# Performance work log

Measured on AMD Instinct MI355X. Metric: run time of the kernel, lower is better.

The kernel has to match this reference:

```python
import jax, jax.numpy as jnp
import numpy as np

B, H, KVH, D, HID = 32, 32, 8, 128, 4096
WIN, MAX_SEQ = 4096, 4096
START_POS = 3000
CURRENT_POS = 3000  # circular index into sliding-window cache

def nearest_32(n):
    return ((n + 31) // 32) * 32

PAD_L = min(nearest_32(START_POS + 1), WIN)  # 3008

def setup_inputs() -> dict:
    key = jax.random.key(0)
    k1, k2, k3 = jax.random.split(key, 3)
    x = jax.random.normal(k1, (1, 1, B, HID), jnp.float32) * 0.02
    wqkv = jax.random.normal(k2, (HID, (H + 2 * KVH) * D), jnp.float32) * 0.02
    wo = jax.random.normal(k3, (HID, HID), jnp.float32) * 0.02
    cache_k = jnp.zeros((B, KVH, WIN, D), jnp.float32)
    cache_v = jnp.zeros((B, KVH, WIN, D), jnp.float32)
    # RoPE tables (rotate-half convention, cos/sin of shape [max_seq_len, head_dim])
    inv_freq = 1.0 / (10000.0 ** (jnp.arange(0, D, 2, dtype=jnp.float32) / D))
    t = jnp.arange(MAX_SEQ, dtype=jnp.float32)
    freqs = jnp.outer(t, inv_freq)                      # [S, D/2]
    emb = jnp.concatenate([freqs, freqs], axis=-1)      # [S, D]
    cos_cached = jnp.cos(emb)
    sin_cached = jnp.sin(emb)
    # additive mask: 0 for valid cache positions (<= start_pos), -1e9 for tile padding
    pos = jnp.arange(PAD_L)
    row = jnp.where(pos <= START_POS, 0.0, -1e9).astype(jnp.float32)
    attn_mask = jnp.broadcast_to(row, (1, H, B, PAD_L))
    return {"x": x, "wqkv": wqkv, "wo": wo, "cache_k": cache_k, "cache_v": cache_v,
            "cos_cached": cos_cached, "sin_cached": sin_cached, "attn_mask": attn_mask,
            "start_pos": START_POS, "current_pos": CURRENT_POS}

def _rotate_half(u):
    return jnp.concatenate([-u[..., D // 2:], u[..., :D // 2]], axis=-1)

def reference(x, wqkv, wo, cache_k, cache_v, cos_cached, sin_cached, attn_mask,
              start_pos, current_pos):
    # fused QKV projection: x is (1,1,B,HID) decode token
    xqkv = x[0, 0] @ wqkv                               # [B, (H+2KVH)*D]
    q = xqkv[:, :H * D].reshape(B, H, D)
    k = xqkv[:, H * D:(H + KVH) * D].reshape(B, KVH, D)
    v = xqkv[:, (H + KVH) * D:].reshape(B, KVH, D)
    # RoPE at position start_pos
    cos = cos_cached[start_pos]                         # [D]
    sin = sin_cached[start_pos]
    q = q * cos + _rotate_half(q) * sin
    k = k * cos + _rotate_half(k) * sin
    # sliding-window circular KV-cache update at current_pos
    cache_k = cache_k.at[:, :, current_pos, :].set(k)
    cache_v = cache_v.at[:, :, current_pos, :].set(v)
    keys = cache_k[:, :, :PAD_L, :]                     # [B, KVH, L, D]
    vals = cache_v[:, :, :PAD_L, :]
    # grouped-query attention
    G = H // KVH
    qg = q.reshape(B, KVH, G, D)
    scores = jnp.einsum('bkgd,bkld->bkgl', qg, keys) / jnp.sqrt(jnp.float32(D))
    mask = jnp.transpose(attn_mask[0], (1, 0, 2)).reshape(B, KVH, G, PAD_L)
    probs = jax.nn.softmax(scores + mask, axis=-1)
    ctx = jnp.einsum('bkgl,bkld->bkgd', probs, vals).reshape(B, H * D)
    dense = ctx @ wo                                    # [B, HID]
    return dense.reshape(1, 1, B, HID)
```

## Files before the change

### kernel.cpp

```cpp
#include <hip/hip_runtime.h>
#include <hip/hip_bf16.h>

#define B 32
#define H 32
#define KVH 8
#define D 128
#define HID 4096
#define NQKV 6144
#define WIN 4096
#define PADL_MAX 3008
#define KS1 16
#define KS4 32

#define OFF_XT   0
#define OFF_P1   131072
#define OFF_QR   (OFF_P1 + KS1*B*NQKV)
#define OFF_KR   (OFF_QR + B*H*D)
#define OFF_VV   (OFF_KR + B*KVH*D)
#define OFF_CTXT (OFF_VV + B*KVH*D)
#define OFF_P4   (OFF_CTXT + B*H*D)

__global__ __launch_bounds__(1024) void k_transpose(const float* __restrict__ x,
                                                    float* __restrict__ xT) {
  __shared__ float t[32][33];
  const int k0 = blockIdx.x * 32;
  const int r = threadIdx.x >> 5, i = threadIdx.x & 31;
  t[r][i] = x[r * HID + k0 + i];
  __syncthreads();
  xT[(k0 + r) * 32 + i] = t[i][r];
}

__global__ __launch_bounds__(256) void k_qkv(const float* __restrict__ xT,
                                             const float* __restrict__ wqkv,
                                             float* __restrict__ P1) {
  __shared__ float xs[256 * 32];
  const int ct = blockIdx.x, ks = blockIdx.y;
  const int tid = threadIdx.x;
  const int col = ct * 256 + tid;
  const int k0 = ks * 256;
  for (int i = tid; i < 256 * 32; i += 256) xs[i] = xT[k0 * 32 + i];
  __syncthreads();
  float acc[32];
#pragma unroll
  for (int b = 0; b < 32; ++b) acc[b] = 0.f;
  const float* wp = wqkv + (size_t)k0 * NQKV + col;
  for (int kk = 0; kk < 256; ++kk) {
    const float w = wp[(size_t)kk * NQKV];
    const float* xr = xs + kk * 32;
#pragma unroll
    for (int b = 0; b < 32; b += 4) {
      const float4 xv = *(const float4*)(xr + b);
      acc[b + 0] = fmaf(xv.x, w, acc[b + 0]);
      acc[b + 1] = fmaf(xv.y, w, acc[b + 1]);
      acc[b + 2] = fmaf(xv.z, w, acc[b + 2]);
      acc[b + 3] = fmaf(xv.w, w, acc[b + 3]);
    }
  }
  float* op = P1 + (size_t)ks * (B * NQKV) + col;
#pragma unroll
  for (int b = 0; b < 32; ++b) op[(size_t)b * NQKV] = acc[b];
}

__global__ __launch_bounds__(256) void k_rope_reduce(const float* __restrict__ P1,
                                                     const float* __restrict__ cosc,
                                                     const float* __restrict__ sinc,
                                                     const int* __restrict__ spp,
                                                     float* __restrict__ qr,
                                                     float* __restrict__ kr,
                                                     float* __restrict__ vv) {
  const int t = blockIdx.x * 256 + threadIdx.x;
  const int sp = *spp;
  if (t < B * (H + KVH) * 64) {
    const int b = t / ((H + KVH) * 64);
    const int r = t % ((H + KVH) * 64);
    const int h = r >> 6;
    const int d = r & 63;
    const int base = b * NQKV + h * D + d;
    float sA = 0.f, sB = 0.f;
#pragma unroll
    for (int s = 0; s < KS1; ++s) {
      sA += P1[(size_t)s * (B * NQKV) + base];
      sB += P1[(size_t)s * (B * NQKV) + base + 64];
    }
    const float cA = cosc[sp * D + d],     snA = sinc[sp * D + d];
    const float cB = cosc[sp * D + d + 64], snB = sinc[sp * D + d + 64];
    const float oA = sA * cA - sB * snA;
    const float oB = sB * cB + sA * snB;
    if (h < H) {
      qr[b * (H * D) + h * D + d] = oA;
      qr[b * (H * D) + h * D + d + 64] = oB;
    } else {
      const int kvh = h - H;
      kr[b * (KVH * D) + kvh * D + d] = oA;
      kr[b * (KVH * D) + kvh * D + d + 64] = oB;
    }
  } else {
    const int i = t - B * (H + KVH) * 64;
    const int b = i >> 10, c = i & 1023;
    float s = 0.f;
#pragma unroll
    for (int ss = 0; ss < KS1; ++ss)
      s += P1[(size_t)ss * (B * NQKV) + b * NQKV + (H + KVH) * D + c];
    vv[i] = s;
  }
}

__global__ __launch_bounds__(1024) void k_attn(const float* __restrict__ cache_k,
                                               const float* __restrict__ cache_v,
                                               const float* __restrict__ qr,
                                               const float* __restrict__ kr,
                                               const float* __restrict__ vv,
                                               const int* __restrict__ spp,
                                               const int* __restrict__ cpp,
                                               float* __restrict__ ctxT) {
  __shared__ float sl[4 * PADL_MAX];
  __shared__ float red[16];
  __shared__ float mg[4], inv[4];
  const int b = blockIdx.x >> 3, kv = blockIdx.x & 7;
  const int sp = *spp, cp = *cpp;
  const int L = sp;
  const int tid = threadIdx.x;
  const int wave = tid >> 6, lane = tid & 63;
  const int half = lane >> 5, j = lane & 31;
  const size_t kvbase = (size_t)(b * KVH + kv) * WIN * D;
  const float scale = 0.08838834764831845f;

  float4 ql[4];
#pragma unroll
  for (int g = 0; g < 4; ++g) {
    float4 q4 = *(const float4*)(qr + b * (H * D) + (kv * 4 + g) * D + 4 * j);
    ql[g] = make_float4(q4.x * scale, q4.y * scale, q4.z * scale, q4.w * scale);
  }

  const int NP = L / 2;
  for (int p = wave; p <= NP; p += 16) {
    const int l = 2 * p + half;
    if (l <= L) {
      const float* kp = (l == cp) ? (kr + (b * KVH + kv) * D)
                                  : (cache_k + kvbase + (size_t)l * D);
      const float4 k4 = *(const float4*)(kp + 4 * j);
#pragma unroll
      for (int g = 0; g < 4; ++g) {
        float s = ql[g].x * k4.x + ql[g].y * k4.y + ql[g].z * k4.z + ql[g].w * k4.w;
#pragma unroll
        for (int m = 1; m <= 16; m <<= 1) s += __shfl_xor(s, m);
        if (j == 0) sl[g * PADL_MAX + l] = s;
      }
    }
  }
  __syncthreads();

  {
    const int g = tid >> 8, i = tid & 255, w4 = (tid >> 6) & 3;
    float m = -1e30f;
    for (int l = i; l <= L; l += 256) m = fmaxf(m, sl[g * PADL_MAX + l]);
#pragma unroll
    for (int mm = 1; mm <= 32; mm <<= 1) m = fmaxf(m, __shfl_xor(m, mm));
    if (lane == 0) red[g * 4 + w4] = m;
    __syncthreads();
    if (i == 0)
      mg[g] = fmaxf(fmaxf(red[g * 4], red[g * 4 + 1]),
                    fmaxf(red[g * 4 + 2], red[g * 4 + 3]));
    __syncthreads();
    const float mgv = mg[g];
    float psum = 0.f;
    for (int l = i; l <= L; l += 256) {
      const float e = __expf(sl[g * PADL_MAX + l] - mgv);
      sl[g * PADL_MAX + l] = e;
      psum += e;
    }
#pragma unroll
    for (int mm = 1; mm <= 32; mm <<= 1) psum += __shfl_xor(psum, mm);
    if (lane == 0) red[g * 4 + w4] = psum;
    __syncthreads();
    if (i == 0)
      inv[g] = 1.f / (red[g * 4] + red[g * 4 + 1] + red[g * 4 + 2] + red[g * 4 + 3]);
    __syncthreads();
  }

  float o[4][4];
#pragma unroll
  for (int g = 0; g < 4; ++g)
#pragma unroll
    for (int c = 0; c < 4; ++c) o[g][c] = 0.f;
  for (int p = wave; p <= NP; p += 16) {
    const int l = 2 * p + half;
    if (l <= L) {
      const float* vp = (l == cp) ? (vv + (b * KVH + kv) * D)
                                  : (cache_v + kvbase + (size_t)l * D);
      const float4 v4 = *(const float4*)(vp + 4 * j);
#pragma unroll
      for (int g = 0; g < 4; ++g) {
        const float e = sl[g * PADL_MAX + l];
        o[g][0] = fmaf(e, v4.x, o[g][0]);
        o[g][1] = fmaf(e, v4.y, o[g][1]);
        o[g][2] = fmaf(e, v4.z, o[g][2]);
        o[g][3] = fmaf(e, v4.w, o[g][3]);
      }
    }
  }
#pragma unroll
  for (int g = 0; g < 4; ++g)
#pragma unroll
    for (int c = 0; c < 4; ++c) o[g][c] += __shfl_xor(o[g][c], 32);

  __syncthreads();
  if (lane < 32) {
#pragma unroll
    for (int g = 0; g < 4; ++g)
      *(float4*)&sl[wave * 512 + g * 128 + 4 * j] =
          make_float4(o[g][0], o[g][1], o[g][2], o[g][3]);
  }
  __syncthreads();
  if (tid < 512) {
    const int g = tid >> 7, d = tid & 127;
    float a = 0.f;
#pragma unroll
    for (int w = 0; w < 16; ++w) a += sl[w * 512 + g * 128 + d];
    a *= inv[g];
    ctxT[(size_t)((kv * 4 + g) * D + d) * B + b] = a;
  }
}

__global__ __launch_bounds__(256) void k_out(const float* __restrict__ ctxT,
                                             const float* __restrict__ wo,
                                             float* __restrict__ P4) {
  __shared__ float cs[128 * 32];
  const int ct = blockIdx.x, ks = blockIdx.y;
  const int tid = threadIdx.x;
  const int col = ct * 256 + tid;
  const int k0 = ks * 128;
  for (int i = tid; i < 128 * 32; i += 256) cs[i] = ctxT[k0 * 32 + i];
  __syncthreads();
  float acc[32];
#pragma unroll
  for (int b = 0; b < 32; ++b) acc[b] = 0.f;
  const float* wp = wo + (size_t)k0 * HID + col;
  for (int kk = 0; kk < 128; ++kk) {
    const float w = wp[(size_t)kk * HID];
    const float* xr = cs + kk * 32;
#pragma unroll
    for (int b = 0; b < 32; b += 4) {
      const float4 xv = *(const float4*)(xr + b);
      acc[b + 0] = fmaf(xv.x, w, acc[b + 0]);
      acc[b + 1] = fmaf(xv.y, w, acc[b + 1]);
      acc[b + 2] = fmaf(xv.z, w, acc[b + 2]);
      acc[b + 3] = fmaf(xv.w, w, acc[b + 3]);
    }
  }
  float* op = P4 + (size_t)ks * (B * HID) + col;
#pragma unroll
  for (int b = 0; b < 32; ++b) op[(size_t)b * HID] = acc[b];
}

__global__ __launch_bounds__(256) void k_final(const float* __restrict__ P4,
                                               float* __restrict__ out) {
  const int e = blockIdx.x * 256 + threadIdx.x;
  float s = 0.f;
#pragma unroll
  for (int ss = 0; ss < KS4; ++ss) s += P4[(size_t)ss * (B * HID) + e];
  out[e] = s;
}

extern "C" void kernel_launch(void* const* d_in, const int* in_sizes, int n_in,
                              void* d_out, int out_size, void* d_ws, size_t ws_size,
                              hipStream_t stream) {
  const float* x       = (const float*)d_in[0];
  const float* wqkv    = (const float*)d_in[1];
  const float* wo      = (const float*)d_in[2];
  const float* cache_k = (const float*)d_in[3];
  const float* cache_v = (const float*)d_in[4];
  const float* cosc    = (const float*)d_in[5];
  const float* sinc    = (const float*)d_in[6];
  const int* spp       = (const int*)d_in[8];
  const int* cpp       = (const int*)d_in[9];
  float* ws = (float*)d_ws;

  k_transpose<<<128, 1024, 0, stream>>>(x, ws + OFF_XT);
  k_qkv<<<dim3(24, 16), 256, 0, stream>>>(ws + OFF_XT, wqkv, ws + OFF_P1);
  k_rope_reduce<<<448, 256, 0, stream>>>(ws + OFF_P1, cosc, sinc, spp,
                                         ws + OFF_QR, ws + OFF_KR, ws + OFF_VV);
  k_attn<<<256, 1024, 0, stream>>>(cache_k, cache_v, ws + OFF_QR, ws + OFF_KR,
                                   ws + OFF_VV, spp, cpp, ws + OFF_CTXT);
  k_out<<<dim3(16, 32), 256, 0, stream>>>(ws + OFF_CTXT, wo, ws + OFF_P4);
  k_final<<<512, 256, 0, stream>>>(ws + OFF_P4, (float*)d_out);
}
```

Before: 1.178 ms.

## Drop transpose kernel, read activations directly in GEMVs, restructure QK scoring

Removes the separate x transpose kernel and the shared-memory staging in the QKV and output projections. Each thread now computes two columns with float2 weight loads and reads activations straight from global memory as wave-uniform broadcast loads. The split-K count for QKV is raised to 32 and the grids are resized to match. The attention QK phase is changed so 8 lanes cooperate per key row with q held in registers, which cuts the shuffle reduction from 5 steps to 3 per score. The trade-off is more partial-sum traffic from the larger split-K and more register pressure from the 2x32 accumulators.

```diff
diff --git a/kernel.cpp b/kernel.cpp
--- a/kernel.cpp
+++ b/kernel.cpp
@@ -9,56 +9,39 @@
 #define NQKV 6144
 #define WIN 4096
 #define PADL_MAX 3008
-#define KS1 16
+#define KS1 32
 #define KS4 32
 
-#define OFF_XT   0
-#define OFF_P1   131072
+#define OFF_P1   0
 #define OFF_QR   (OFF_P1 + KS1*B*NQKV)
 #define OFF_KR   (OFF_QR + B*H*D)
 #define OFF_VV   (OFF_KR + B*KVH*D)
-#define OFF_CTXT (OFF_VV + B*KVH*D)
-#define OFF_P4   (OFF_CTXT + B*H*D)
-
-__global__ __launch_bounds__(1024) void k_transpose(const float* __restrict__ x,
-                                                    float* __restrict__ xT) {
-  __shared__ float t[32][33];
-  const int k0 = blockIdx.x * 32;
-  const int r = threadIdx.x >> 5, i = threadIdx.x & 31;
-  t[r][i] = x[r * HID + k0 + i];
-  __syncthreads();
-  xT[(k0 + r) * 32 + i] = t[i][r];
-}
-
-__global__ __launch_bounds__(256) void k_qkv(const float* __restrict__ xT,
+#define OFF_CTX  (OFF_VV + B*KVH*D)
+#define OFF_P4   (OFF_CTX + B*H*D)
+
+__global__ __launch_bounds__(256) void k_qkv(const float* __restrict__ x,
                                              const float* __restrict__ wqkv,
                                              float* __restrict__ P1) {
-  __shared__ float xs[256 * 32];
-  const int ct = blockIdx.x, ks = blockIdx.y;
-  const int tid = threadIdx.x;
-  const int col = ct * 256 + tid;
-  const int k0 = ks * 256;
-  for (int i = tid; i < 256 * 32; i += 256) xs[i] = xT[k0 * 32 + i];
-  __syncthreads();
-  float acc[32];
-#pragma unroll
-  for (int b = 0; b < 32; ++b) acc[b] = 0.f;
+  const int ks = blockIdx.y;
+  const int col = blockIdx.x * 512 + threadIdx.x * 2;
+  const int k0 = ks * 128;
+  float2 acc[32];
+#pragma unroll
+  for (int b = 0; b < 32; ++b) acc[b] = make_float2(0.f, 0.f);
   const float* wp = wqkv + (size_t)k0 * NQKV + col;
-  for (int kk = 0; kk < 256; ++kk) {
-    const float w = wp[(size_t)kk * NQKV];
-    const float* xr = xs + kk * 32;
-#pragma unroll
-    for (int b = 0; b < 32; b += 4) {
-      const float4 xv = *(const float4*)(xr + b);
-      acc[b + 0] = fmaf(xv.x, w, acc[b + 0]);
-      acc[b + 1] = fmaf(xv.y, w, acc[b + 1]);
-      acc[b + 2] = fmaf(xv.z, w, acc[b + 2]);
-      acc[b + 3] = fmaf(xv.w, w, acc[b + 3]);
+  for (int kk = 0; kk < 128; ++kk) {
+    const float2 w2 = *(const float2*)(wp + (size_t)kk * NQKV);
+    const int xi = k0 + kk;
+#pragma unroll
+    for (int b = 0; b < 32; ++b) {
+      const float xv = x[b * HID + xi];
+      acc[b].x = fmaf(xv, w2.x, acc[b].x);
+      acc[b].y = fmaf(xv, w2.y, acc[b].y);
     }
   }
   float* op = P1 + (size_t)ks * (B * NQKV) + col;
 #pragma unroll
-  for (int b = 0; b < 32; ++b) op[(size_t)b * NQKV] = acc[b];
+  for (int b = 0; b < 32; ++b) *(float2*)(op + (size_t)b * NQKV) = acc[b];
 }
 
 __global__ __launch_bounds__(256) void k_rope_reduce(const float* __restrict__ P1,
@@ -82,7 +65,7 @@
       sA += P1[(size_t)s * (B * NQKV) + base];
       sB += P1[(size_t)s * (B * NQKV) + base + 64];
     }
-    const float cA = cosc[sp * D + d],     snA = sinc[sp * D + d];
+    const float cA = cosc[sp * D + d],      snA = sinc[sp * D + d];
     const float cB = cosc[sp * D + d + 64], snB = sinc[sp * D + d + 64];
     const float oA = sA * cA - sB * snA;
     const float oB = sB * cB + sA * snB;
@@ -112,8 +95,9 @@
                                                const float* __restrict__ vv,
                                                const int* __restrict__ spp,
                                                const int* __restrict__ cpp,
-                                               float* __restrict__ ctxT) {
+                                               float* __restrict__ ctx) {
   __shared__ float sl[4 * PADL_MAX];
+  __shared__ float sq[4 * D];
   __shared__ float red[16];
   __shared__ float mg[4], inv[4];
   const int b = blockIdx.x >> 3, kv = blockIdx.x & 7;
@@ -121,30 +105,47 @@
   const int L = sp;
   const int tid = threadIdx.x;
   const int wave = tid >> 6, lane = tid & 63;
-  const int half = lane >> 5, j = lane & 31;
   const size_t kvbase = (size_t)(b * KVH + kv) * WIN * D;
   const float scale = 0.08838834764831845f;
 
-  float4 ql[4];
-#pragma unroll
-  for (int g = 0; g < 4; ++g) {
-    float4 q4 = *(const float4*)(qr + b * (H * D) + (kv * 4 + g) * D + 4 * j);
-    ql[g] = make_float4(q4.x * scale, q4.y * scale, q4.z * scale, q4.w * scale);
-  }
-
-  const int NP = L / 2;
-  for (int p = wave; p <= NP; p += 16) {
-    const int l = 2 * p + half;
+  if (tid < 512) sq[tid] = qr[b * (H * D) + kv * 4 * D + tid] * scale;
+  __syncthreads();
+
+  const int grp = tid >> 3;
+  const int c = tid & 7;
+  float4 ql[4][4];
+#pragma unroll
+  for (int g = 0; g < 4; ++g)
+#pragma unroll
+    for (int t = 0; t < 4; ++t)
+      ql[g][t] = *(const float4*)(sq + g * D + (t * 8 + c) * 4);
+
+  for (int l0 = 0; l0 < 3072; l0 += 128) {
+    const int l = l0 + grp;
     if (l <= L) {
       const float* kp = (l == cp) ? (kr + (b * KVH + kv) * D)
                                   : (cache_k + kvbase + (size_t)l * D);
-      const float4 k4 = *(const float4*)(kp + 4 * j);
-#pragma unroll
-      for (int g = 0; g < 4; ++g) {
-        float s = ql[g].x * k4.x + ql[g].y * k4.y + ql[g].z * k4.z + ql[g].w * k4.w;
-#pragma unroll
-        for (int m = 1; m <= 16; m <<= 1) s += __shfl_xor(s, m);
-        if (j == 0) sl[g * PADL_MAX + l] = s;
+      float s0 = 0.f, s1 = 0.f, s2 = 0.f, s3 = 0.f;
+#pragma unroll
+      for (int t = 0; t < 4; ++t) {
+        const float4 k4 = *(const float4*)(kp + (t * 8 + c) * 4);
+        s0 += ql[0][t].x * k4.x + ql[0][t].y * k4.y + ql[0][t].z * k4.z + ql[0][t].w * k4.w;
+        s1 += ql[1][t].x * k4.x + ql[1][t].y * k4.y + ql[1][t].z * k4.z + ql[1][t].w * k4.w;
+        s2 += ql[2][t].x * k4.x + ql[2][t].y * k4.y + ql[2][t].z * k4.z + ql[2][t].w * k4.w;
+        s3 += ql[3][t].x * k4.x + ql[3][t].y * k4.y + ql[3][t].z * k4.z + ql[3][t].w * k4.w;
+      }
+#pragma unroll
+      for (int m = 1; m <= 4; m <<= 1) {
+        s0 += __shfl_xor(s0, m);
+        s1 += __shfl_xor(s1, m);
+        s2 += __shfl_xor(s2, m);
+        s3 += __shfl_xor(s3, m);
+      }
+      if (c == 0) {
+        sl[0 * PADL_MAX + l] = s0;
+        sl[1 * PADL_MAX + l] = s1;
+        sl[2 * PADL_MAX + l] = s2;
+        sl[3 * PADL_MAX + l] = s3;
       }
     }
   }
@@ -178,11 +179,13 @@
     __syncthreads();
   }
 
+  const int half = lane >> 5, j = lane & 31;
   float o[4][4];
 #pragma unroll
   for (int g = 0; g < 4; ++g)
 #pragma unroll
-    for (int c = 0; c < 4; ++c) o[g][c] = 0.f;
+    for (int cc = 0; cc < 4; ++cc) o[g][cc] = 0.f;
+  const int NP = L / 2;
   for (int p = wave; p <= NP; p += 16) {
     const int l = 2 * p + half;
     if (l <= L) {
@@ -202,7 +205,7 @@
 #pragma unroll
   for (int g = 0; g < 4; ++g)
 #pragma unroll
-    for (int c = 0; c < 4; ++c) o[g][c] += __shfl_xor(o[g][c], 32);
+    for (int cc = 0; cc < 4; ++cc) o[g][cc] += __shfl_xor(o[g][cc], 32);
 
   __syncthreads();
   if (lane < 32) {
@@ -218,39 +221,33 @@
 #pragma unroll
     for (int w = 0; w < 16; ++w) a += sl[w * 512 + g * 128 + d];
     a *= inv[g];
-    ctxT[(size_t)((kv * 4 + g) * D + d) * B + b] = a;
-  }
-}
-
-__global__ __launch_bounds__(256) void k_out(const float* __restrict__ ctxT,
+    ctx[b * (H * D) + (kv * 4 + g) * D + d] = a;
+  }
+}
+
+__global__ __launch_bounds__(256) void k_out(const float* __restrict__ ctx,
                                              const float* __restrict__ wo,
                                              float* __restrict__ P4) {
-  __shared__ float cs[128 * 32];
-  const int ct = blockIdx.x, ks = blockIdx.y;
-  const int tid = threadIdx.x;
-  const int col = ct * 256 + tid;
+  const int ks = blockIdx.y;
+  const int col = blockIdx.x * 512 + threadIdx.x * 2;
   const int k0 = ks * 128;
-  for (int i = tid; i < 128 * 32; i += 256) cs[i] = ctxT[k0 * 32 + i];
-  __syncthreads();
-  float acc[32];
-#pragma unroll
-  for (int b = 0; b < 32; ++b) acc[b] = 0.f;
+  float2 acc[32];
+#pragma unroll
+  for (int b = 0; b < 32; ++b) acc[b] = make_float2(0.f, 0.f);
   const float* wp = wo + (size_t)k0 * HID + col;
   for (int kk = 0; kk < 128; ++kk) {
-    const float w = wp[(size_t)kk * HID];
-    const float* xr = cs + kk * 32;
-#pragma unroll
-    for (int b = 0; b < 32; b += 4) {
-      const float4 xv = *(const float4*)(xr + b);
-      acc[b + 0] = fmaf(xv.x, w, acc[b + 0]);
-      acc[b + 1] = fmaf(xv.y, w, acc[b + 1]);
-      acc[b + 2] = fmaf(xv.z, w, acc[b + 2]);
-      acc[b + 3] = fmaf(xv.w, w, acc[b + 3]);
+    const float2 w2 = *(const float2*)(wp + (size_t)kk * HID);
+    const int xi = k0 + kk;
+#pragma unroll
+    for (int b = 0; b < 32; ++b) {
+      const float xv = ctx[b * HID + xi];
+      acc[b].x = fmaf(xv, w2.x, acc[b].x);
+      acc[b].y = fmaf(xv, w2.y, acc[b].y);
     }
   }
   float* op = P4 + (size_t)ks * (B * HID) + col;
 #pragma unroll
-  for (int b = 0; b < 32; ++b) op[(size_t)b * HID] = acc[b];
+  for (int b = 0; b < 32; ++b) *(float2*)(op + (size_t)b * HID) = acc[b];
 }
 
 __global__ __launch_bounds__(256) void k_final(const float* __restrict__ P4,
@@ -276,12 +273,11 @@
   const int* cpp       = (const int*)d_in[9];
   float* ws = (float*)d_ws;
 
-  k_transpose<<<128, 1024, 0, stream>>>(x, ws + OFF_XT);
-  k_qkv<<<dim3(24, 16), 256, 0, stream>>>(ws + OFF_XT, wqkv, ws + OFF_P1);
+  k_qkv<<<dim3(12, 32), 256, 0, stream>>>(x, wqkv, ws + OFF_P1);
   k_rope_reduce<<<448, 256, 0, stream>>>(ws + OFF_P1, cosc, sinc, spp,
                                          ws + OFF_QR, ws + OFF_KR, ws + OFF_VV);
   k_attn<<<256, 1024, 0, stream>>>(cache_k, cache_v, ws + OFF_QR, ws + OFF_KR,
-                                   ws + OFF_VV, spp, cpp, ws + OFF_CTXT);
-  k_out<<<dim3(16, 32), 256, 0, stream>>>(ws + OFF_CTXT, wo, ws + OFF_P4);
+                                   ws + OFF_VV, spp, cpp, ws + OFF_CTX);
+  k_out<<<dim3(8, 32), 256, 0, stream>>>(ws + OFF_CTX, wo, ws + OFF_P4);
   k_final<<<512, 256, 0, stream>>>(ws + OFF_P4, (float*)d_out);
 }
```

Result: no change. 1.167 ms (-0.9%).
